# Kernel tuning notes

Measured on AMD Instinct MI355X. Metric: run time of the kernel, lower is better.

Reference implementation:

```python
import jax, jax.numpy as jnp
import numpy as np

D_MODEL = 1024
NUM_HEADS = 16
D_HEAD = D_MODEL // NUM_HEADS  # 64, used only as softmax scale
DFF = 4096
EPS = 1e-6


def _layernorm(x, gamma, beta):
    mu = jnp.mean(x, axis=-1, keepdims=True)
    var = jnp.mean(jnp.square(x - mu), axis=-1, keepdims=True)
    return (x - mu) * jax.lax.rsqrt(var + EPS) * gamma + beta


def _mha(q_in, kv, score, Wq, bq, Wk, bk, Wv, bv, Wo, bo):
    # q_in: [B,Sq,d]; kv: [Sv,d] (broadcast over batch, mirroring unsqueeze(0))
    Q = q_in @ Wq.T + bq                      # [B,Sq,d]
    K = kv @ Wk.T + bk                        # [Sv,d]
    V = kv @ Wv.T + bv                        # [Sv,d]
    scores = (jnp.einsum('bqd,kd->bqk', Q, K) + score) / jnp.sqrt(
        jnp.asarray(D_HEAD, dtype=jnp.float32))
    w = jax.nn.softmax(scores, axis=-1)       # [B,Sq,Sv]
    out = jnp.einsum('bqk,kd->bqd', w, V)     # [B,Sq,d]
    return out @ Wo.T + bo


def setup_inputs() -> dict:
    key = jax.random.key(0)
    ks = jax.random.split(key, 20)
    B, Sq, Sv = 4, 2048, 196
    s = 0.02
    inp = {
        'text_tensor': jax.random.normal(ks[0], (B, Sq, D_MODEL), jnp.float32),
        'visual_tensor': jax.random.normal(ks[1], (Sv, D_MODEL), jnp.float32),
        'score_matrix': jax.random.normal(ks[2], (B, Sq, Sv), jnp.float32),
        'text_tensor2': jax.random.normal(ks[3], (B, Sq, D_MODEL), jnp.float32),
        'visual_tensor2': jax.random.normal(ks[4], (Sv, D_MODEL), jnp.float32),
        'score_matrix2': jax.random.normal(ks[5], (B, Sq, Sv), jnp.float32),
        'Wq': jax.random.normal(ks[6], (D_MODEL, D_MODEL), jnp.float32) * s,
        'bq': jnp.zeros((D_MODEL,), jnp.float32),
        'Wk': jax.random.normal(ks[7], (D_MODEL, D_MODEL), jnp.float32) * s,
        'bk': jnp.zeros((D_MODEL,), jnp.float32),
        'Wv': jax.random.normal(ks[8], (D_MODEL, D_MODEL), jnp.float32) * s,
        'bv': jnp.zeros((D_MODEL,), jnp.float32),
        'Wo': jax.random.normal(ks[9], (D_MODEL, D_MODEL), jnp.float32) * s,
        'bo': jnp.zeros((D_MODEL,), jnp.float32),
        'W1': jax.random.normal(ks[10], (DFF, D_MODEL), jnp.float32) * s,
        'b1': jnp.zeros((DFF,), jnp.float32),
        'W2': jax.random.normal(ks[11], (D_MODEL, DFF), jnp.float32) * s,
        'b2': jnp.zeros((D_MODEL,), jnp.float32),
        'g1': jnp.ones((D_MODEL,), jnp.float32),
        'be1': jnp.zeros((D_MODEL,), jnp.float32),
        'g2': jnp.ones((D_MODEL,), jnp.float32),
        'be2': jnp.zeros((D_MODEL,), jnp.float32),
    }
    return inp


def reference(text_tensor, visual_tensor, score_matrix,
              text_tensor2, visual_tensor2, score_matrix2,
              Wq, bq, Wk, bk, Wv, bv, Wo, bo,
              W1, b1, W2, b2, g1, be1, g2, be2):
    # Branch 1 (dropout is identity in eval mode)
    a1 = _mha(text_tensor, visual_tensor, score_matrix,
              Wq, bq, Wk, bk, Wv, bv, Wo, bo)
    out1 = _layernorm(text_tensor + a1, g1, be1)
    # Branch 2 (shared attention weights, same layernorm1)
    a2 = _mha(text_tensor2, visual_tensor2, score_matrix2,
              Wq, bq, Wk, bk, Wv, bv, Wo, bo)
    out2 = _layernorm(text_tensor2 + a2, g1, be1)
    # Concat along features then MaxPool1d(kernel=2, stride=2) over last dim
    concat = jnp.concatenate([out1, out2], axis=2)       # [B,Sq,2d]
    B, Sq, _ = concat.shape
    pooled = jnp.max(concat.reshape(B, Sq, D_MODEL, 2), axis=-1)  # [B,Sq,d]
    # FFN + residual + layernorm2
    ffn = jax.nn.relu(pooled @ W1.T + b1) @ W2.T + b2
    return _layernorm(pooled + ffn, g2, be2)
```

## Files before the change

### kernel.cpp

```cpp
#include <hip/hip_runtime.h>
#include <hip/hip_bf16.h>
#include <cstdint>
#include <type_traits>

typedef unsigned short u16;
typedef __bf16 bf16x8 __attribute__((ext_vector_type(8)));
typedef float f32x4 __attribute__((ext_vector_type(4)));

#define LN_EPS 1e-6f

enum { BIAS_NONE = 0, BIAS_COL = 1, BIAS_ROW = 2, BIAS_COL2 = 3 };

__device__ __forceinline__ float b2f(u16 h) {
  union { unsigned u; float f; } v;
  v.u = ((unsigned)h) << 16;
  return v.f;
}
__device__ __forceinline__ u16 f2b(float x) {
  return __bfloat16_as_ushort(__float2bfloat16(x));
}

__device__ __forceinline__ void gld_lds16(const void* g, void* l) {
  __builtin_amdgcn_global_load_lds(
      (const __attribute__((address_space(1))) void*)g,
      (__attribute__((address_space(3))) void*)l, 16, 0, 0);
}

__device__ __forceinline__ void st8(float4 a, float4 b, u16* dst) {
  u16 t[8] = {f2b(a.x), f2b(a.y), f2b(a.z), f2b(a.w),
              f2b(b.x), f2b(b.y), f2b(b.z), f2b(b.w)};
  *reinterpret_cast<uint4*>(dst) = *reinterpret_cast<const uint4*>(t);
}

__device__ __forceinline__ void stage8_cvt(const float* src, size_t off,
                                           u16* dst) {
  const float* p = src + off;
  st8(*reinterpret_cast<const float4*>(p),
      *reinterpret_cast<const float4*>(p + 4), dst);
}

template <typename OutT, int BIAS, bool RELU, bool A_RAW, bool B_RAW, int TM,
          int TN, int BK, int NT, int LB>
__global__ __launch_bounds__(NT, LB) void gemm_db(
    const void* __restrict__ A, const void* __restrict__ A2,
    const void* __restrict__ B, const void* __restrict__ B2,
    const float* __restrict__ bias, const float* __restrict__ bias2,
    OutT* __restrict__ C, int M, int N, int K, int lda, int ldb, int MA,
    int NB, int ldc, int Msplit, int rowmask, int colsplit) {
  constexpr int SA = (TM * BK) / (NT * 8);
  constexpr int SB = (TN * BK) / (NT * 8);
  constexpr int AI = (NT == 512) ? 2 : ((TM == 128 && TN == 128) ? 4 : 2);
  constexpr int BJ = (TM == 64 && TN == 64) ? 2 : 4;
  __shared__ __align__(16) u16 As[2][TM * BK];
  __shared__ __align__(16) u16 Bs[2][TN * BK];
  const int tid = threadIdx.x;
  const int lane = tid & 63;
  const int wv = tid >> 6;
  int wr, wc;
  if constexpr (NT == 512) {
    wr = (wv & 3) * 32; wc = (wv >> 2) * 64;
  } else if constexpr (TM == 128 && TN == 128) {
    wr = (wv >> 1) * 64; wc = (wv & 1) * 64;
  } else if constexpr (TM == 128 && TN == 64) {
    wr = wv * 32; wc = 0;
  } else {
    wr = (wv >> 1) * 32; wc = (wv & 1) * 32;
  }
  const int mrow = lane & 15;
  const int quad = lane >> 4;

  int bxi = blockIdx.x, byi = blockIdx.y;
  {
    const int gx = (int)gridDim.x;
    const int nwg = gx * (int)gridDim.y;
    if ((nwg & 7) == 0) {
      int wg = byi * gx + bxi;
      wg = (wg & 7) * (nwg >> 3) + (wg >> 3);
      bxi = wg % gx;
      byi = wg / gx;
    }
  }
  const int bm = byi * TM;
  const int bn = bxi * TN;

  f32x4 acc[AI][BJ];
#pragma unroll
  for (int i = 0; i < AI; i++)
#pragma unroll
    for (int j = 0; j < BJ; j++) acc[i][j] = f32x4{0.f, 0.f, 0.f, 0.f};

  const int e0 = tid * 8;
  const int r0t = e0 >> 5;
  const int swc8 = ((((e0 >> 3) & 3) ^ ((r0t >> 1) & 3)) << 3);

  const void* Asrc[SA];
  size_t aoff[SA];
#pragma unroll
  for (int s = 0; s < SA; s++) {
    const int h = (s * NT * 8) / (TM * 32);
    const int rb = ((s * NT * 8) % (TM * 32)) >> 5;
    int ra = bm + rb + r0t;
    if (ra >= MA) ra = MA - 1;
    Asrc[s] = (ra < Msplit) ? A : A2;
    const int rr = (ra < Msplit) ? ra : ra - Msplit;
    aoff[s] = (size_t)rr * lda + h * 32 + swc8;
  }
  const void* Bb = (bm < Msplit) ? B : B2;
  size_t boff[SB];
#pragma unroll
  for (int s = 0; s < SB; s++) {
    const int h = (s * NT * 8) / (TN * 32);
    const int rb = ((s * NT * 8) % (TN * 32)) >> 5;
    int rbn = bn + rb + r0t;
    if (rbn >= NB) rbn = NB - 1;
    boff[s] = (size_t)rbn * ldb + h * 32 + swc8;
  }

#pragma unroll
  for (int s = 0; s < SA; s++) {
    if constexpr (A_RAW) {
      const float* p = (const float*)Asrc[s] + aoff[s];
      st8(*reinterpret_cast<const float4*>(p),
          *reinterpret_cast<const float4*>(p + 4), &As[0][s * NT * 8 + e0]);
    } else {
      gld_lds16((const u16*)Asrc[s] + aoff[s], &As[0][s * NT * 8 + e0]);
    }
  }
#pragma unroll
  for (int s = 0; s < SB; s++) {
    if constexpr (B_RAW) {
      const float* p = (const float*)Bb + boff[s];
      st8(*reinterpret_cast<const float4*>(p),
          *reinterpret_cast<const float4*>(p + 4), &Bs[0][s * NT * 8 + e0]);
    } else {
      gld_lds16((const u16*)Bb + boff[s], &Bs[0][s * NT * 8 + e0]);
    }
  }
  __syncthreads();

  const int so = ((quad ^ ((mrow >> 1) & 3)) << 3);

  int cur = 0;
  for (int k0 = 0; k0 < K; k0 += BK) {
    const int nk = k0 + BK;
    const bool pf = nk < K;
    float4 fA[SA][2], fB[SB][2];
    if (pf) {
#pragma unroll
      for (int s = 0; s < SA; s++) {
        if constexpr (A_RAW) {
          const float* p = (const float*)Asrc[s] + aoff[s] + nk;
          fA[s][0] = *reinterpret_cast<const float4*>(p);
          fA[s][1] = *reinterpret_cast<const float4*>(p + 4);
        } else {
          gld_lds16((const u16*)Asrc[s] + aoff[s] + nk,
                    &As[cur ^ 1][s * NT * 8 + e0]);
        }
      }
#pragma unroll
      for (int s = 0; s < SB; s++) {
        if constexpr (B_RAW) {
          const float* p = (const float*)Bb + boff[s] + nk;
          fB[s][0] = *reinterpret_cast<const float4*>(p);
          fB[s][1] = *reinterpret_cast<const float4*>(p + 4);
        } else {
          gld_lds16((const u16*)Bb + boff[s] + nk,
                    &Bs[cur ^ 1][s * NT * 8 + e0]);
        }
      }
    }
#pragma unroll
    for (int h = 0; h < BK / 32; h++) {
      bf16x8 af[AI], bfm[BJ];
#pragma unroll
      for (int i = 0; i < AI; i++)
        af[i] = *reinterpret_cast<const bf16x8*>(
            &As[cur][h * TM * 32 + (wr + i * 16 + mrow) * 32 + so]);
#pragma unroll
      for (int j = 0; j < BJ; j++)
        bfm[j] = *reinterpret_cast<const bf16x8*>(
            &Bs[cur][h * TN * 32 + (wc + j * 16 + mrow) * 32 + so]);
#pragma unroll
      for (int i = 0; i < AI; i++)
#pragma unroll
        for (int j = 0; j < BJ; j++)
          acc[i][j] = __builtin_amdgcn_mfma_f32_16x16x32_bf16(
              af[i], bfm[j], acc[i][j], 0, 0, 0);
    }
    if (pf) {
      if constexpr (A_RAW) {
#pragma unroll
        for (int s = 0; s < SA; s++)
          st8(fA[s][0], fA[s][1], &As[cur ^ 1][s * NT * 8 + e0]);
      }
      if constexpr (B_RAW) {
#pragma unroll
        for (int s = 0; s < SB; s++)
          st8(fB[s][0], fB[s][1], &Bs[cur ^ 1][s * NT * 8 + e0]);
      }
    }
    __syncthreads();
    cur ^= 1;
  }

  const float* bp = (bm < Msplit) ? bias : bias2;
#pragma unroll
  for (int i = 0; i < AI; i++) {
#pragma unroll
    for (int j = 0; j < BJ; j++) {
#pragma unroll
      for (int r = 0; r < 4; r++) {
        const int gr = bm + wr + i * 16 + quad * 4 + r;
        const int gc = bn + wc + j * 16 + mrow;
        if (gr < M && gc < N) {
          float v = acc[i][j][r];
          if (BIAS == BIAS_COL) v += bp[gc];
          if (BIAS == BIAS_COL2)
            v += (gc < colsplit) ? bias[gc] : bias2[gc - colsplit];
          if (BIAS == BIAS_ROW) v += bp[gr & rowmask];
          if (RELU) v = fmaxf(v, 0.f);
          if constexpr (std::is_same<OutT, float>::value)
            C[(size_t)gr * ldc + gc] = v;
          else
            C[(size_t)gr * ldc + gc] = f2b(v);
        }
      }
    }
  }
}

__global__ __launch_bounds__(256) void cvt3_k(
    const float* __restrict__ s0, u16* __restrict__ d0,
    const float* __restrict__ s1, u16* __restrict__ d1,
    const float* __restrict__ s2, u16* __restrict__ d2, int blocksPer) {
  const int seg = blockIdx.x / blocksPer;
  const int b = blockIdx.x % blocksPer;
  const float* s = (seg == 0) ? s0 : ((seg == 1) ? s1 : s2);
  u16* d = (seg == 0) ? d0 : ((seg == 1) ? d1 : d2);
  const size_t i = ((size_t)b * 256 + threadIdx.x) * 8;
  stage8_cvt(s, i, d + i);
}

__global__ __launch_bounds__(256) void wqt_k(const float* __restrict__ src,
                                             u16* __restrict__ dst) {
  __shared__ float t[64][65];
  const int bx = blockIdx.x;
  const int by = blockIdx.y;
  const int tx = threadIdx.x & 63;
  const int ty = threadIdx.x >> 6;
#pragma unroll
  for (int i = 0; i < 16; i++)
    t[ty * 16 + i][tx] =
        src[(size_t)(by * 64 + ty * 16 + i) * 1024 + bx * 64 + tx];
  __syncthreads();
#pragma unroll
  for (int i = 0; i < 16; i++)
    dst[(size_t)(bx * 64 + ty * 16 + i) * 1024 + by * 64 + tx] =
        f2b(t[tx][ty * 16 + i]);
}

__global__ __launch_bounds__(256) void kb_k(const u16* __restrict__ Kc,
                                            const float* __restrict__ bq,
                                            float* __restrict__ kb, int ld) {
  const int wvi = blockIdx.x * 4 + (threadIdx.x >> 6);
  const int lane = threadIdx.x & 63;
  const int b = wvi / 224, s = wvi % 224;
  float sum = 0.f;
  if (s < 196) {
    const u16* row = Kc + (size_t)(b * 196 + s) * ld;
    for (int j = lane; j < 1024; j += 64) sum += b2f(row[j]) * bq[j];
  }
#pragma unroll
  for (int off = 32; off > 0; off >>= 1) sum += __shfl_xor(sum, off);
  if (lane == 0) kb[wvi] = sum;
}

__global__ __launch_bounds__(256) void softmax_k(
    u16* __restrict__ Sp, const float* __restrict__ sc1,
    const float* __restrict__ sc2) {
  const int row = blockIdx.x * 4 + (threadIdx.x >> 6);
  const int lane = threadIdx.x & 63;
  const float* score = (row < 8192) ? sc1 + (size_t)row * 196
                                    : sc2 + (size_t)(row - 8192) * 196;
  float x[4];
  float mx = -1e30f;
#pragma unroll
  for (int t = 0; t < 4; t++) {
    const int s = lane + 64 * t;
    float v = -1e30f;
    if (s < 196) v = (b2f(Sp[(size_t)row * 224 + s]) + score[s]) * 0.125f;
    x[t] = v;
    mx = fmaxf(mx, v);
  }
#pragma unroll
  for (int off = 32; off > 0; off >>= 1) mx = fmaxf(mx, __shfl_xor(mx, off));
  float sum = 0.f;
#pragma unroll
  for (int t = 0; t < 4; t++) {
    const int s = lane + 64 * t;
    const float e = (s < 196) ? expf(x[t] - mx) : 0.f;
    x[t] = e;
    sum += e;
  }
#pragma unroll
  for (int off = 32; off > 0; off >>= 1) sum += __shfl_xor(sum, off);
  const float inv = 1.f / sum;
#pragma unroll
  for (int t = 0; t < 4; t++) {
    const int s = lane + 64 * t;
    if (s < 224) Sp[(size_t)row * 224 + s] = f2b((s < 196) ? x[t] * inv : 0.f);
  }
}

__global__ __launch_bounds__(256) void ln_pool_k(
    const float* __restrict__ X1, const float* __restrict__ X2,
    const u16* __restrict__ Y, const float* __restrict__ g,
    const float* __restrict__ be, u16* __restrict__ pooled) {
  const int row16 = blockIdx.x;
  const int br = row16 >> 13;
  const int row = row16 & 8191;
  const int tid = threadIdx.x;
  const int lane = tid & 63;
  const int wv = tid >> 6;
  const float* X = (br ? X2 : X1) + (size_t)row * 1024;
  const u16* Yp = Y + (size_t)row16 * 1024;
  __shared__ float red[4];
  float v[4];
  float s = 0.f;
#pragma unroll
  for (int j = 0; j < 4; j++) {
    const float a = X[tid * 4 + j] + b2f(Yp[tid * 4 + j]);
    v[j] = a;
    s += a;
  }
#pragma unroll
  for (int off = 32; off > 0; off >>= 1) s += __shfl_xor(s, off);
  if (lane == 0) red[wv] = s;
  __syncthreads();
  const float mu = (red[0] + red[1] + red[2] + red[3]) * (1.f / 1024.f);
  __syncthreads();
  float var = 0.f;
#pragma unroll
  for (int j = 0; j < 4; j++) {
    const float d = v[j] - mu;
    var += d * d;
  }
#pragma unroll
  for (int off = 32; off > 0; off >>= 1) var += __shfl_xor(var, off);
  if (lane == 0) red[wv] = var;
  __syncthreads();
  var = (red[0] + red[1] + red[2] + red[3]) * (1.f / 1024.f);
  const float rs = rsqrtf(var + LN_EPS);
  float n[4];
#pragma unroll
  for (int j = 0; j < 4; j++)
    n[j] = (v[j] - mu) * rs * g[tid * 4 + j] + be[tid * 4 + j];
  const size_t pb = (size_t)row * 1024 + br * 512 + tid * 2;
  pooled[pb] = f2b(fmaxf(n[0], n[1]));
  pooled[pb + 1] = f2b(fmaxf(n[2], n[3]));
}

__global__ __launch_bounds__(256) void ln_out_k(
    const u16* __restrict__ X, const u16* __restrict__ Y,
    const float* __restrict__ g, const float* __restrict__ be,
    float* __restrict__ out) {
  const int row = blockIdx.x;
  const int tid = threadIdx.x;
  const int lane = tid & 63;
  const int wv = tid >> 6;
  __shared__ float red[4];
  float v[4];
  float s = 0.f;
  const size_t base = (size_t)row * 1024 + tid * 4;
#pragma unroll
  for (int j = 0; j < 4; j++) {
    const float a = b2f(X[base + j]) + b2f(Y[base + j]);
    v[j] = a;
    s += a;
  }
#pragma unroll
  for (int off = 32; off > 0; off >>= 1) s += __shfl_xor(s, off);
  if (lane == 0) red[wv] = s;
  __syncthreads();
  const float mu = (red[0] + red[1] + red[2] + red[3]) * (1.f / 1024.f);
  __syncthreads();
  float var = 0.f;
#pragma unroll
  for (int j = 0; j < 4; j++) {
    const float d = v[j] - mu;
    var += d * d;
  }
#pragma unroll
  for (int off = 32; off > 0; off >>= 1) var += __shfl_xor(var, off);
  if (lane == 0) red[wv] = var;
  __syncthreads();
  var = (red[0] + red[1] + red[2] + red[3]) * (1.f / 1024.f);
  const float rs = rsqrtf(var + LN_EPS);
#pragma unroll
  for (int j = 0; j < 4; j++)
    out[base + j] = (v[j] - mu) * rs * g[tid * 4 + j] + be[tid * 4 + j];
}

extern "C" void kernel_launch(void* const* d_in, const int* in_sizes, int n_in,
                              void* d_out, int out_size, void* d_ws,
                              size_t ws_size, hipStream_t stream) {
  const size_t MB = 1ull << 20;
  if (ws_size < 61 * MB) return;

  const float* text1 = (const float*)d_in[0];
  const float* vis1 = (const float*)d_in[1];
  const float* sc1 = (const float*)d_in[2];
  const float* text2 = (const float*)d_in[3];
  const float* vis2 = (const float*)d_in[4];
  const float* sc2 = (const float*)d_in[5];
  const float* Wq = (const float*)d_in[6];
  const float* bq = (const float*)d_in[7];
  const float* Wk = (const float*)d_in[8];
  const float* bk = (const float*)d_in[9];
  const float* Wv = (const float*)d_in[10];
  const float* bv = (const float*)d_in[11];
  const float* Wo = (const float*)d_in[12];
  const float* bo = (const float*)d_in[13];
  const float* W1 = (const float*)d_in[14];
  const float* b1 = (const float*)d_in[15];
  const float* W2 = (const float*)d_in[16];
  const float* b2 = (const float*)d_in[17];
  const float* g1 = (const float*)d_in[18];
  const float* be1 = (const float*)d_in[19];
  const float* g2 = (const float*)d_in[20];
  const float* be2 = (const float*)d_in[21];

  const int D = 1024, Sv = 196, SvP = 224, DFF = 4096;
  const int M2 = 16384;
  char* w = (char*)d_ws;
  u16* pooled = (u16*)(w + 0 * MB);
  u16* Wkb = (u16*)(w + 16 * MB);
  u16* Wvb = (u16*)(w + 18 * MB);
  u16* Wob = (u16*)(w + 20 * MB);
  u16* WqT = (u16*)(w + 22 * MB);
  u16* KVcat = (u16*)(w + 24 * MB);
  u16* K2cat = (u16*)(w + 26 * MB);
  u16* VWoT = (u16*)(w + 27 * MB);
  float* kb = (float*)(w + 28 * MB);
  u16* Spcat = (u16*)(w + 29 * MB);
  u16* Ocat = (u16*)d_out;
  u16* H = (u16*)(w + 16 * MB);
  u16* F = (u16*)(w + 48 * MB);
  u16* W1b = (u16*)((char*)d_out + 16 * MB);
  u16* W2b = (u16*)((char*)d_out + 24 * MB);

  auto grid = [](int m, int n, int tm, int tn) {
    return dim3((unsigned)((n + tn - 1) / tn), (unsigned)((m + tm - 1) / tm));
  };

  cvt3_k<<<dim3(3 * 512), 256, 0, stream>>>(Wk, Wkb, Wv, Wvb, Wo, Wob, 512);
  wqt_k<<<dim3(16, 16), 256, 0, stream>>>(Wq, WqT);

  gemm_db<u16, BIAS_COL2, false, true, false, 64, 64, 32, 256, 8>
      <<<grid(2 * Sv, 2 * D, 64, 64), 256, 0, stream>>>(
          vis1, vis2, Wkb, Wkb, bk, bv, KVcat, 2 * Sv, 2 * D, D, D, D, 2 * Sv,
          2 * D, 2 * D, Sv, 0, D);
  gemm_db<u16, BIAS_NONE, false, false, false, 64, 64, 32, 256, 8>
      <<<grid(2 * Sv, D, 64, 64), 256, 0, stream>>>(
          KVcat, KVcat, WqT, WqT, nullptr, nullptr, K2cat, 2 * Sv, D, D, 2 * D,
          D, 2 * Sv, D, D, 2 * Sv, 0, 0);
  kb_k<<<dim3(112), 256, 0, stream>>>(KVcat, bq, kb, 2 * D);
  gemm_db<u16, BIAS_COL, false, true, false, 64, 64, 32, 256, 8>
      <<<grid(M2, Sv, 64, 64), 256, 0, stream>>>(
          text1, text2, K2cat, K2cat + (size_t)Sv * D, kb, kb + SvP, Spcat, M2,
          Sv, D, D, D, M2, Sv, SvP, 8192, 0, 0);
  softmax_k<<<dim3(M2 / 4), 256, 0, stream>>>(Spcat, sc1, sc2);
  gemm_db<u16, BIAS_ROW, false, false, false, 64, 64, 32, 256, 8>
      <<<grid(2 * D, SvP, 64, 64), 256, 0, stream>>>(
          Wob, Wob, KVcat + D, KVcat + (size_t)Sv * 2 * D + D, bo, bo, VWoT,
          2 * D, SvP, D, D, 2 * D, 2 * D, Sv, SvP, D, D - 1, 0);
  gemm_db<u16, BIAS_NONE, false, false, false, 64, 64, 32, 256, 8>
      <<<grid(M2, D, 64, 64), 256, 0, stream>>>(
          Spcat, Spcat + (size_t)8192 * SvP, VWoT, VWoT + (size_t)D * SvP,
          nullptr, nullptr, Ocat, M2, D, SvP, SvP, SvP, M2, D, D, 8192, 0, 0);
  ln_pool_k<<<dim3(M2), 256, 0, stream>>>(text1, text2, Ocat, g1, be1, pooled);

  cvt3_k<<<dim3(2 * 2048), 256, 0, stream>>>(W1, W1b, W2, W2b, W2, W2b, 2048);

  for (int c = 0; c < 2; ++c) {
    const int r0 = c * 4096, rows = 4096;
    gemm_db<u16, BIAS_COL, true, false, false, 128, 128, 32, 256, 4>
        <<<grid(rows, DFF, 128, 128), 256, 0, stream>>>(
            pooled + (size_t)r0 * D, pooled + (size_t)r0 * D, W1b, W1b, b1, b1,
            H, rows, DFF, D, D, D, rows, DFF, DFF, rows, 0, 0);
    gemm_db<u16, BIAS_COL, false, false, false, 64, 64, 64, 256, 5>
        <<<grid(rows, D, 64, 64), 256, 0, stream>>>(
            H, H, W2b, W2b, b2, b2, F, rows, D, DFF, DFF, DFF, rows, D, D,
            rows, 0, 0);
    ln_out_k<<<dim3(rows), 256, 0, stream>>>(
        pooled + (size_t)r0 * D, F, g2, be2, (float*)d_out + (size_t)r0 * D);
  }
}
```

Before: 534.9 us.

## Split FFN over hidden dim with fp32 accumulation and raw fp32 weights

Restructures the FFN so that instead of two row chunks, the full 8192 rows are processed in two halves of the 4096-wide hidden dimension. Each half goes through W1 then W2, with the second W2 GEMM accumulating into an fp32 output buffer via a new read-modify-write epilogue. The W1/W2 bf16 conversion kernel is dropped and the fp32 weights are read raw inside the GEMMs. The final layernorm now runs once, reading fp32 F. This trades the separate weight conversion and bf16 F round-trip for extra fp32 traffic on the output and in-GEMM conversion of B.

```diff
diff --git a/kernel.cpp b/kernel.cpp
--- a/kernel.cpp
+++ b/kernel.cpp
@@ -40,7 +40,7 @@
 }
 
 template <typename OutT, int BIAS, bool RELU, bool A_RAW, bool B_RAW, int TM,
-          int TN, int BK, int NT, int LB>
+          int TN, int BK, int NT, int LB, bool CACC>
 __global__ __launch_bounds__(NT, LB) void gemm_db(
     const void* __restrict__ A, const void* __restrict__ A2,
     const void* __restrict__ B, const void* __restrict__ B2,
@@ -218,6 +218,7 @@
           if (BIAS == BIAS_COL2)
             v += (gc < colsplit) ? bias[gc] : bias2[gc - colsplit];
           if (BIAS == BIAS_ROW) v += bp[gr & rowmask];
+          if (CACC) v += (float)C[(size_t)gr * ldc + gc];
           if (RELU) v = fmaxf(v, 0.f);
           if constexpr (std::is_same<OutT, float>::value)
             C[(size_t)gr * ldc + gc] = v;
@@ -360,8 +361,8 @@
   pooled[pb + 1] = f2b(fmaxf(n[2], n[3]));
 }
 
-__global__ __launch_bounds__(256) void ln_out_k(
-    const u16* __restrict__ X, const u16* __restrict__ Y,
+__global__ __launch_bounds__(256) void ln_out_f_k(
+    const u16* __restrict__ X, const float* __restrict__ Y,
     const float* __restrict__ g, const float* __restrict__ be,
     float* __restrict__ out) {
   const int row = blockIdx.x;
@@ -374,7 +375,7 @@
   const size_t base = (size_t)row * 1024 + tid * 4;
 #pragma unroll
   for (int j = 0; j < 4; j++) {
-    const float a = b2f(X[base + j]) + b2f(Y[base + j]);
+    const float a = b2f(X[base + j]) + Y[base + j];
     v[j] = a;
     s += a;
   }
@@ -445,9 +446,7 @@
   u16* Spcat = (u16*)(w + 29 * MB);
   u16* Ocat = (u16*)d_out;
   u16* H = (u16*)(w + 16 * MB);
-  u16* F = (u16*)(w + 48 * MB);
-  u16* W1b = (u16*)((char*)d_out + 16 * MB);
-  u16* W2b = (u16*)((char*)d_out + 24 * MB);
+  float* Fp = (float*)d_out;
 
   auto grid = [](int m, int n, int tm, int tn) {
     return dim3((unsigned)((n + tn - 1) / tn), (unsigned)((m + tm - 1) / tm));
@@ -456,43 +455,48 @@
   cvt3_k<<<dim3(3 * 512), 256, 0, stream>>>(Wk, Wkb, Wv, Wvb, Wo, Wob, 512);
   wqt_k<<<dim3(16, 16), 256, 0, stream>>>(Wq, WqT);
 
-  gemm_db<u16, BIAS_COL2, false, true, false, 64, 64, 32, 256, 8>
+  gemm_db<u16, BIAS_COL2, false, true, false, 64, 64, 32, 256, 8, false>
       <<<grid(2 * Sv, 2 * D, 64, 64), 256, 0, stream>>>(
           vis1, vis2, Wkb, Wkb, bk, bv, KVcat, 2 * Sv, 2 * D, D, D, D, 2 * Sv,
           2 * D, 2 * D, Sv, 0, D);
-  gemm_db<u16, BIAS_NONE, false, false, false, 64, 64, 32, 256, 8>
+  gemm_db<u16, BIAS_NONE, false, false, false, 64, 64, 32, 256, 8, false>
       <<<grid(2 * Sv, D, 64, 64), 256, 0, stream>>>(
           KVcat, KVcat, WqT, WqT, nullptr, nullptr, K2cat, 2 * Sv, D, D, 2 * D,
           D, 2 * Sv, D, D, 2 * Sv, 0, 0);
   kb_k<<<dim3(112), 256, 0, stream>>>(KVcat, bq, kb, 2 * D);
-  gemm_db<u16, BIAS_COL, false, true, false, 64, 64, 32, 256, 8>
+  gemm_db<u16, BIAS_COL, false, true, false, 64, 64, 32, 256, 8, false>
       <<<grid(M2, Sv, 64, 64), 256, 0, stream>>>(
           text1, text2, K2cat, K2cat + (size_t)Sv * D, kb, kb + SvP, Spcat, M2,
           Sv, D, D, D, M2, Sv, SvP, 8192, 0, 0);
   softmax_k<<<dim3(M2 / 4), 256, 0, stream>>>(Spcat, sc1, sc2);
-  gemm_db<u16, BIAS_ROW, false, false, false, 64, 64, 32, 256, 8>
+  gemm_db<u16, BIAS_ROW, false, false, false, 64, 64, 32, 256, 8, false>
       <<<grid(2 * D, SvP, 64, 64), 256, 0, stream>>>(
           Wob, Wob, KVcat + D, KVcat + (size_t)Sv * 2 * D + D, bo, bo, VWoT,
           2 * D, SvP, D, D, 2 * D, 2 * D, Sv, SvP, D, D - 1, 0);
-  gemm_db<u16, BIAS_NONE, false, false, false, 64, 64, 32, 256, 8>
+  gemm_db<u16, BIAS_NONE, false, false, false, 64, 64, 32, 256, 8, false>
       <<<grid(M2, D, 64, 64), 256, 0, stream>>>(
           Spcat, Spcat + (size_t)8192 * SvP, VWoT, VWoT + (size_t)D * SvP,
           nullptr, nullptr, Ocat, M2, D, SvP, SvP, SvP, M2, D, D, 8192, 0, 0);
   ln_pool_k<<<dim3(M2), 256, 0, stream>>>(text1, text2, Ocat, g1, be1, pooled);
 
-  cvt3_k<<<dim3(2 * 2048), 256, 0, stream>>>(W1, W1b, W2, W2b, W2, W2b, 2048);
-
   for (int c = 0; c < 2; ++c) {
-    const int r0 = c * 4096, rows = 4096;
-    gemm_db<u16, BIAS_COL, true, false, false, 128, 128, 32, 256, 4>
-        <<<grid(rows, DFF, 128, 128), 256, 0, stream>>>(
-            pooled + (size_t)r0 * D, pooled + (size_t)r0 * D, W1b, W1b, b1, b1,
-            H, rows, DFF, D, D, D, rows, DFF, DFF, rows, 0, 0);
-    gemm_db<u16, BIAS_COL, false, false, false, 64, 64, 64, 256, 5>
-        <<<grid(rows, D, 64, 64), 256, 0, stream>>>(
-            H, H, W2b, W2b, b2, b2, F, rows, D, DFF, DFF, DFF, rows, D, D,
-            rows, 0, 0);
-    ln_out_k<<<dim3(rows), 256, 0, stream>>>(
-        pooled + (size_t)r0 * D, F, g2, be2, (float*)d_out + (size_t)r0 * D);
-  }
-}
+    const size_t wo1 = (size_t)c * 2048 * D;
+    gemm_db<u16, BIAS_COL, true, false, true, 128, 128, 32, 256, 4, false>
+        <<<grid(8192, 2048, 128, 128), 256, 0, stream>>>(
+            pooled, pooled, W1 + wo1, W1 + wo1, b1 + c * 2048, b1 + c * 2048,
+            H, 8192, 2048, D, D, D, 8192, 2048, 2048, 8192, 0, 0);
+    if (c == 0) {
+      gemm_db<float, BIAS_COL, false, false, true, 64, 64, 32, 256, 8, false>
+          <<<grid(8192, D, 64, 64), 256, 0, stream>>>(
+              H, H, W2, W2, b2, b2, Fp, 8192, D, 2048, 2048, DFF, 8192, D, D,
+              8192, 0, 0);
+    } else {
+      gemm_db<float, BIAS_NONE, false, false, true, 64, 64, 32, 256, 8, true>
+          <<<grid(8192, D, 64, 64), 256, 0, stream>>>(
+              H, H, W2 + 2048, W2 + 2048, nullptr, nullptr, Fp, 8192, D, 2048,
+              2048, DFF, 8192, D, D, 8192, 0, 0);
+    }
+  }
+  ln_out_f_k<<<dim3(8192), 256, 0, stream>>>(pooled, Fp, g2, be2,
+                                             (float*)d_out);
+}
```

After: 636.3 us. +19.0%, slower.
